# Optimization experiments

Hardware: AMD Instinct MI355X
Metric: run time of the kernel (lower is better)

Reference implementation:

```python
import jax, jax.numpy as jnp
import numpy as np

N_TOKENS = 8192
D_MODEL = 1024
D_HIDDEN = 4096
N_EXPERTS = 8
TOP_K = 2


def setup_inputs() -> dict:
    key = jax.random.key(0)
    ks = jax.random.split(key, 7)
    s = 0.02
    return {
        "x": jax.random.normal(ks[0], (N_TOKENS, D_MODEL), dtype=jnp.float32),
        "gate_w": jax.random.normal(ks[1], (D_MODEL, N_EXPERTS), dtype=jnp.float32) * s,
        "gate_b": jnp.zeros((N_EXPERTS,), dtype=jnp.float32),
        "w1": jax.random.normal(ks[2], (N_EXPERTS, D_MODEL, D_HIDDEN), dtype=jnp.float32) * s,
        "b1": jnp.zeros((N_EXPERTS, D_HIDDEN), dtype=jnp.float32),
        "w2": jax.random.normal(ks[3], (N_EXPERTS, D_HIDDEN, D_MODEL), dtype=jnp.float32) * s,
        "b2": jnp.zeros((N_EXPERTS, D_MODEL), dtype=jnp.float32),
    }


def reference(x, gate_w, gate_b, w1, b1, w2, b2):
    # Gating: softmax over experts, then top-k routing
    gate_scores = jax.nn.softmax(x @ gate_w + gate_b, axis=-1)        # [N, E]
    topk_vals, topk_idx = jax.lax.top_k(gate_scores, TOP_K)          # [N, K]

    # Combine weights: sum of topk_vals scattered to expert slots
    onehot = jax.nn.one_hot(topk_idx, N_EXPERTS, dtype=x.dtype)      # [N, K, E]
    combine = jnp.einsum('nk,nke->ne', topk_vals, onehot)            # [N, E]

    # Dense expert evaluation (math identical to masked dispatch: unselected
    # experts receive weight 0 in `combine`).
    h = jax.nn.relu(jnp.einsum('nd,edh->neh', x, w1) + b1)           # [N, E, H]
    expert_out = jnp.einsum('neh,ehd->ned', h, w2) + b2              # [N, E, D]
    output = jnp.einsum('ned,ne->nd', expert_out, combine)           # [N, D]

    # Load-balancing loss from routing counts
    load = jnp.sum(onehot, axis=(0, 1))                              # [E]
    load_balancing_loss = jnp.sum((load / jnp.sum(load)) ** 2)
    return output, load_balancing_loss
```

## Files before the change

kernel.cpp:

```cpp
#include <hip/hip_runtime.h>

#define D_MODEL   1024
#define D_HIDDEN  4096
#define N_EXPERTS 8
#define N_TOKENS  8192
#define NASSIGN   (N_TOKENS * 2)
#define PADCAP    (NASSIGN + N_EXPERTS * 128)
#define ROWT      (PADCAP / 128)

typedef unsigned short u16;
typedef __bf16 bf16x8 __attribute__((ext_vector_type(8)));
typedef float  f32x4  __attribute__((ext_vector_type(4)));

__device__ __forceinline__ u16 f2bf(float f) {
  union { float f; unsigned u; } c; c.f = f;
  unsigned u = c.u;
  u = (u + 0x7fffu + ((u >> 16) & 1u)) >> 16;
  return (u16)u;
}

__device__ __forceinline__ void async16(const void* g, void* l) {
  __builtin_amdgcn_global_load_lds(
      (const __attribute__((address_space(1))) unsigned int*)g,
      (__attribute__((address_space(3))) unsigned int*)l, 16, 0, 0);
}

__global__ __launch_bounds__(256) void gating_kernel(
    const float* __restrict__ x, const float* __restrict__ gw,
    const float* __restrict__ gb, int* __restrict__ counts,
    int* __restrict__ tok_idx, float* __restrict__ tok_w)
{
  const int n = blockIdx.x * 4 + (threadIdx.x >> 6);
  const int lane = threadIdx.x & 63;
  float acc[8] = {0.f,0.f,0.f,0.f,0.f,0.f,0.f,0.f};
  for (int d = lane; d < D_MODEL; d += 64) {
    float xv = x[(size_t)n * D_MODEL + d];
    const float4* g = (const float4*)&gw[d * 8];
    float4 g0 = g[0], g1 = g[1];
    acc[0] += xv * g0.x; acc[1] += xv * g0.y; acc[2] += xv * g0.z; acc[3] += xv * g0.w;
    acc[4] += xv * g1.x; acc[5] += xv * g1.y; acc[6] += xv * g1.z; acc[7] += xv * g1.w;
  }
  for (int off = 32; off; off >>= 1)
    #pragma unroll
    for (int e = 0; e < 8; ++e) acc[e] += __shfl_xor(acc[e], off, 64);
  if (lane == 0) {
    float l[8], p[8];
    float m = -1e30f;
    for (int e = 0; e < 8; ++e) { l[e] = acc[e] + gb[e]; m = fmaxf(m, l[e]); }
    float s = 0.f;
    for (int e = 0; e < 8; ++e) { p[e] = expf(l[e] - m); s += p[e]; }
    float inv = 1.f / s;
    for (int e = 0; e < 8; ++e) p[e] *= inv;
    int i0 = 0;
    for (int e = 1; e < 8; ++e) if (p[e] > p[i0]) i0 = e;
    int i1 = (i0 == 0) ? 1 : 0;
    for (int e = 0; e < 8; ++e) if (e != i0 && p[e] > p[i1]) i1 = e;
    tok_idx[2 * n]     = i0;  tok_idx[2 * n + 1] = i1;
    tok_w[2 * n]       = p[i0]; tok_w[2 * n + 1] = p[i1];
    atomicAdd(&counts[i0], 1);
    atomicAdd(&counts[i1], 1);
  }
}

__global__ void finalize_routing(const int* __restrict__ counts,
                                 int* __restrict__ offsets,
                                 float* __restrict__ out_loss)
{
  int off = 0;
  for (int e = 0; e < 8; ++e) {
    offsets[e] = off;
    off += ((counts[e] + 127) >> 7) << 7;
  }
  offsets[8] = off;
  float loss = 0.f;
  for (int e = 0; e < 8; ++e) {
    float f = (float)counts[e] * (1.f / (float)NASSIGN);
    loss += f * f;
  }
  *out_loss = loss;
}

__global__ __launch_bounds__(256) void scatter_kernel(
    const int* __restrict__ tok_idx, const float* __restrict__ tok_w,
    const int* __restrict__ offsets, int* __restrict__ cursors,
    int* __restrict__ assign_token, float* __restrict__ assign_w,
    int* __restrict__ tok_pos)
{
  const int n = blockIdx.x * 256 + threadIdx.x;
  #pragma unroll
  for (int k = 0; k < 2; ++k) {
    int e = tok_idx[n * 2 + k];
    int pos = offsets[e] + atomicAdd(&cursors[e], 1);
    assign_token[pos] = n;
    assign_w[pos] = tok_w[n * 2 + k];
    tok_pos[n * 2 + k] = pos;
  }
}

__global__ __launch_bounds__(256) void convert_x_kernel(
    const float* __restrict__ x, u16* __restrict__ xb)
{
  size_t i = ((size_t)blockIdx.x * 256 + threadIdx.x) * 4;
  float4 v = *(const float4*)&x[i];
  unsigned lo = (unsigned)f2bf(v.x) | ((unsigned)f2bf(v.y) << 16);
  unsigned hi = (unsigned)f2bf(v.z) | ((unsigned)f2bf(v.w) << 16);
  uint2 o; o.x = lo; o.y = hi;
  *(uint2*)&xb[i] = o;
}

__global__ __launch_bounds__(256) void transpose_cvt_kernel(
    const float* __restrict__ in, u16* __restrict__ out, int R, int C)
{
  const int e = blockIdx.z;
  const int c0 = blockIdx.x * 32, r0 = blockIdx.y * 32;
  __shared__ float tile[32][33];
  const int tx = threadIdx.x & 31, ty = threadIdx.x >> 5;
  const float* ip = in + (size_t)e * R * C;
  u16* op = out + (size_t)e * R * C;
  #pragma unroll
  for (int i = 0; i < 4; ++i)
    tile[ty + i * 8][tx] = ip[(size_t)(r0 + ty + i * 8) * C + c0 + tx];
  __syncthreads();
  #pragma unroll
  for (int i = 0; i < 4; ++i)
    op[(size_t)(c0 + ty + i * 8) * R + r0 + tx] = f2bf(tile[tx][ty + i * 8]);
}


__global__ __launch_bounds__(512, 1) void gemm1_kernel(
    const u16* __restrict__ xb, const u16* __restrict__ w1t,
    const float* __restrict__ b1, const int* __restrict__ assign_token,
    const int* __restrict__ offsets, u16* __restrict__ hbuf)
{
  const int rt = blockIdx.x, ct = blockIdx.y;
  if (rt * 128 >= offsets[8]) return;
  int e = 0;
  while (offsets[e + 1] <= rt * 128) ++e;

  __shared__ __align__(16) u16 smem[49152];
  const int tid = threadIdx.x;
  const int wave = tid >> 6, lane = tid & 63;

  const int arow0 = tid >> 3;
  const int aslot0 = (tid & 7) ^ (arow0 & 7);
  const int ac1 = tid + 512;
  const int arow1 = ac1 >> 3;
  const int aslot1 = (ac1 & 7) ^ (arow1 & 7);
  const long aBase0 = (long)assign_token[rt * 128 + arow0] * D_MODEL + aslot0 * 8;
  const long aBase1 = (long)assign_token[rt * 128 + arow1] * D_MODEL + aslot1 * 8;

  long bBase[4];
  #pragma unroll
  for (int k = 0; k < 4; ++k) {
    int c = tid + k * 512;
    int r = c >> 3, s = (c & 7) ^ (r & 7);
    bBase[k] = ((long)e * D_HIDDEN + ct * 256 + r) * D_MODEL + s * 8;
  }

  const int wr = (wave >> 2) * 64;
  const int wc = (wave & 3) * 64;
  f32x4 acc[4][4];
  #pragma unroll
  for (int i = 0; i < 4; ++i)
    #pragma unroll
    for (int j = 0; j < 4; ++j) acc[i][j] = (f32x4){0.f, 0.f, 0.f, 0.f};

  int aro[4], asz[4], bro[4], bsz[4];
  #pragma unroll
  for (int i = 0; i < 4; ++i) {
    int row = wr + i * 16 + (lane & 15);
    aro[i] = row * 64; asz[i] = row & 7;
    int col = wc + i * 16 + (lane & 15);
    bro[i] = col * 64; bsz[i] = col & 7;
  }
  const int lh = lane >> 4;

  #define STG1(p, k0) do { \
    u16* A_ = smem + (p) * 8192; \
    u16* B_ = smem + 16384 + (p) * 16384; \
    async16(xb  + aBase0   + (k0), A_ + wave * 512); \
    async16(xb  + aBase1   + (k0), A_ + 4096 + wave * 512); \
    async16(w1t + bBase[0] + (k0), B_ + wave * 512); \
    async16(w1t + bBase[1] + (k0), B_ + 4096 + wave * 512); \
    async16(w1t + bBase[2] + (k0), B_ + 8192 + wave * 512); \
    async16(w1t + bBase[3] + (k0), B_ + 12288 + wave * 512); \
  } while (0)

  const int NT = D_MODEL / 64;
  STG1(0, 0);
  __syncthreads();
  for (int t = 0; t < NT; ++t) {
    if (t + 1 < NT) STG1((t + 1) & 1, (t + 1) * 64);
    const u16* A = smem + (t & 1) * 8192;
    const u16* B = smem + 16384 + (t & 1) * 16384;
    bf16x8 a[2][4], b[2][4];
    #pragma unroll
    for (int i = 0; i < 4; ++i) {
      a[0][i] = *(const bf16x8*)&A[aro[i] + ((lh       ^ asz[i]) * 8)];
      a[1][i] = *(const bf16x8*)&A[aro[i] + (((4 | lh) ^ asz[i]) * 8)];
      b[0][i] = *(const bf16x8*)&B[bro[i] + ((lh       ^ bsz[i]) * 8)];
      b[1][i] = *(const bf16x8*)&B[bro[i] + (((4 | lh) ^ bsz[i]) * 8)];
    }
    __builtin_amdgcn_s_setprio(1);
    #pragma unroll
    for (int i = 0; i < 4; ++i)
      #pragma unroll
      for (int j = 0; j < 4; ++j) {
        acc[i][j] = __builtin_amdgcn_mfma_f32_16x16x32_bf16(a[0][i], b[0][j], acc[i][j], 0, 0, 0);
        acc[i][j] = __builtin_amdgcn_mfma_f32_16x16x32_bf16(a[1][i], b[1][j], acc[i][j], 0, 0, 0);
      }
    __builtin_amdgcn_s_setprio(0);
    __syncthreads();
  }
  #undef STG1

  float bias[4];
  #pragma unroll
  for (int j = 0; j < 4; ++j)
    bias[j] = b1[(size_t)e * D_HIDDEN + ct * 256 + wc + j * 16 + (lane & 15)];

  u16* Hs = smem;
  #pragma unroll
  for (int i = 0; i < 4; ++i)
    #pragma unroll
    for (int j = 0; j < 4; ++j)
      #pragma unroll
      for (int r = 0; r < 4; ++r) {
        int rl = wr + i * 16 + ((lane >> 4) * 4) + r;
        int cl = wc + j * 16 + (lane & 15);
        Hs[rl * 256 + cl] = f2bf(fmaxf(acc[i][j][r] + bias[j], 0.f));
      }
  __syncthreads();
  #pragma unroll
  for (int t = 0; t < 8; ++t) {
    int cc = tid + t * 512;
    int row = cc >> 5, cs = cc & 31;
    *(uint4*)&hbuf[((size_t)(rt * 128 + row)) * D_HIDDEN + ct * 256 + cs * 8] =
        *(const uint4*)&Hs[row * 256 + cs * 8];
  }
}

template <bool EO>
__global__ __launch_bounds__(512, 1) void gemm2_kernel(
    const u16* __restrict__ hbuf, const u16* __restrict__ w2t,
    const float* __restrict__ b2, const int* __restrict__ assign_token,
    const float* __restrict__ assign_w, const int* __restrict__ offsets,
    float* __restrict__ dst)
{
  const int rt = blockIdx.x, ct = blockIdx.y;
  if (rt * 128 >= offsets[8]) return;
  int e = 0;
  while (offsets[e + 1] <= rt * 128) ++e;

  __shared__ __align__(16) u16 smem[49152];
  __shared__ int tokS[128];
  __shared__ float wS[128];

  const int tid = threadIdx.x;
  const int wave = tid >> 6, lane = tid & 63;
  if (tid < 128) {
    tokS[tid] = assign_token[rt * 128 + tid];
    wS[tid] = assign_w[rt * 128 + tid];
  }

  const int arow0 = tid >> 3;
  const int aslot0 = (tid & 7) ^ (arow0 & 7);
  const int ac1 = tid + 512;
  const int arow1 = ac1 >> 3;
  const int aslot1 = (ac1 & 7) ^ (arow1 & 7);
  const long aBase0 = ((long)(rt * 128 + arow0)) * D_HIDDEN + aslot0 * 8;
  const long aBase1 = ((long)(rt * 128 + arow1)) * D_HIDDEN + aslot1 * 8;

  long bBase[4];
  #pragma unroll
  for (int k = 0; k < 4; ++k) {
    int c = tid + k * 512;
    int r = c >> 3, s = (c & 7) ^ (r & 7);
    bBase[k] = ((long)e * D_MODEL + ct * 256 + r) * D_HIDDEN + s * 8;
  }

  const int wr = (wave >> 2) * 64;
  const int wc = (wave & 3) * 64;
  f32x4 acc[4][4];
  #pragma unroll
  for (int i = 0; i < 4; ++i)
    #pragma unroll
    for (int j = 0; j < 4; ++j) acc[i][j] = (f32x4){0.f, 0.f, 0.f, 0.f};

  int aro[4], asz[4], bro[4], bsz[4];
  #pragma unroll
  for (int i = 0; i < 4; ++i) {
    int row = wr + i * 16 + (lane & 15);
    aro[i] = row * 64; asz[i] = row & 7;
    int col = wc + i * 16 + (lane & 15);
    bro[i] = col * 64; bsz[i] = col & 7;
  }
  const int lh = lane >> 4;

  #define STG2(p, k0) do { \
    u16* A_ = smem + (p) * 8192; \
    u16* B_ = smem + 16384 + (p) * 16384; \
    async16(hbuf + aBase0   + (k0), A_ + wave * 512); \
    async16(hbuf + aBase1   + (k0), A_ + 4096 + wave * 512); \
    async16(w2t  + bBase[0] + (k0), B_ + wave * 512); \
    async16(w2t  + bBase[1] + (k0), B_ + 4096 + wave * 512); \
    async16(w2t  + bBase[2] + (k0), B_ + 8192 + wave * 512); \
    async16(w2t  + bBase[3] + (k0), B_ + 12288 + wave * 512); \
  } while (0)

  const int NT = D_HIDDEN / 64;
  STG2(0, 0);
  __syncthreads();
  for (int t = 0; t < NT; ++t) {
    if (t + 1 < NT) STG2((t + 1) & 1, (t + 1) * 64);
    const u16* A = smem + (t & 1) * 8192;
    const u16* B = smem + 16384 + (t & 1) * 16384;
    bf16x8 a[2][4], b[2][4];
    #pragma unroll
    for (int i = 0; i < 4; ++i) {
      a[0][i] = *(const bf16x8*)&A[aro[i] + ((lh       ^ asz[i]) * 8)];
      a[1][i] = *(const bf16x8*)&A[aro[i] + (((4 | lh) ^ asz[i]) * 8)];
      b[0][i] = *(const bf16x8*)&B[bro[i] + ((lh       ^ bsz[i]) * 8)];
      b[1][i] = *(const bf16x8*)&B[bro[i] + (((4 | lh) ^ bsz[i]) * 8)];
    }
    __builtin_amdgcn_s_setprio(1);
    #pragma unroll
    for (int i = 0; i < 4; ++i)
      #pragma unroll
      for (int j = 0; j < 4; ++j) {
        acc[i][j] = __builtin_amdgcn_mfma_f32_16x16x32_bf16(a[0][i], b[0][j], acc[i][j], 0, 0, 0);
        acc[i][j] = __builtin_amdgcn_mfma_f32_16x16x32_bf16(a[1][i], b[1][j], acc[i][j], 0, 0, 0);
      }
    __builtin_amdgcn_s_setprio(0);
    __syncthreads();
  }
  #undef STG2

  float bias[4];
  #pragma unroll
  for (int j = 0; j < 4; ++j)
    bias[j] = b2[(size_t)e * D_MODEL + ct * 256 + wc + j * 16 + (lane & 15)];

  #pragma unroll
  for (int i = 0; i < 4; ++i)
    #pragma unroll
    for (int r = 0; r < 4; ++r) {
      int rl = wr + i * 16 + ((lane >> 4) * 4) + r;
      float wgt = wS[rl];
      if (EO) {
        size_t row = (size_t)(rt * 128 + rl);
        #pragma unroll
        for (int j = 0; j < 4; ++j) {
          float v = (acc[i][j][r] + bias[j]) * wgt;
          dst[row * D_MODEL + ct * 256 + wc + j * 16 + (lane & 15)] = v;
        }
      } else {
        int tok = tokS[rl];
        #pragma unroll
        for (int j = 0; j < 4; ++j) {
          float v = (acc[i][j][r] + bias[j]) * wgt;
          atomicAdd(&dst[(size_t)tok * D_MODEL + ct * 256 + wc + j * 16 + (lane & 15)], v);
        }
      }
    }
}

__global__ __launch_bounds__(256) void combine_kernel(
    const float* __restrict__ eo, const int* __restrict__ tok_pos,
    float* __restrict__ out)
{
  int idx = blockIdx.x * 256 + threadIdx.x;
  int n = idx >> 8;
  int c = (idx & 255) * 4;
  int p0 = tok_pos[2 * n], p1 = tok_pos[2 * n + 1];
  float4 a = *(const float4*)&eo[(size_t)p0 * D_MODEL + c];
  float4 b = *(const float4*)&eo[(size_t)p1 * D_MODEL + c];
  float4 o; o.x = a.x + b.x; o.y = a.y + b.y; o.z = a.z + b.z; o.w = a.w + b.w;
  *(float4*)&out[(size_t)n * D_MODEL + c] = o;
}

__global__ __launch_bounds__(256) void moe_fallback_kernel(
    const float* __restrict__ x, const float* __restrict__ w1,
    const float* __restrict__ b1, const float* __restrict__ w2,
    const float* __restrict__ b2, const int* __restrict__ tok_idx,
    const float* __restrict__ tok_w, float* __restrict__ out)
{
  const int a = blockIdx.x;
  const int n = a >> 1, slot = a & 1;
  const int e = tok_idx[n * 2 + slot];
  const float wgt = tok_w[n * 2 + slot];
  __shared__ float xs[D_MODEL];
  __shared__ float hs[D_HIDDEN];
  const int tid = threadIdx.x;
  for (int d = tid; d < D_MODEL; d += 256) xs[d] = x[(size_t)n * D_MODEL + d];
  __syncthreads();
  for (int h = tid; h < D_HIDDEN; h += 256) {
    float acc = b1[(size_t)e * D_HIDDEN + h];
    for (int d = 0; d < D_MODEL; ++d)
      acc += xs[d] * w1[((size_t)e * D_MODEL + d) * D_HIDDEN + h];
    hs[h] = fmaxf(acc, 0.f);
  }
  __syncthreads();
  for (int d = tid; d < D_MODEL; d += 256) {
    float acc = b2[(size_t)e * D_MODEL + d];
    for (int h = 0; h < D_HIDDEN; ++h)
      acc += hs[h] * w2[((size_t)e * D_HIDDEN + h) * D_MODEL + d];
    atomicAdd(&out[(size_t)n * D_MODEL + d], wgt * acc);
  }
}

extern "C" void kernel_launch(void* const* d_in, const int* in_sizes, int n_in,
                              void* d_out, int out_size, void* d_ws, size_t ws_size,
                              hipStream_t stream) {
  const float* x      = (const float*)d_in[0];
  const float* gate_w = (const float*)d_in[1];
  const float* gate_b = (const float*)d_in[2];
  const float* w1     = (const float*)d_in[3];
  const float* b1     = (const float*)d_in[4];
  const float* w2     = (const float*)d_in[5];
  const float* b2     = (const float*)d_in[6];
  float* out = (float*)d_out;

  char* ws = (char*)d_ws;
  int*   counts       = (int*)(ws + 0);
  int*   cursors      = (int*)(ws + 32);
  int*   offsets      = (int*)(ws + 64);
  int*   tok_idx      = (int*)(ws + 256);
  float* tok_w        = (float*)(ws + 65792);
  int*   tok_pos      = (int*)(ws + 131328);
  int*   assign_token = (int*)(ws + 196864);
  float* assign_w     = (float*)(ws + 266496);
  const size_t X0 = 336128;
  u16* xb   = (u16*)(ws + X0);
  u16* w1t  = (u16*)(ws + X0 + 16777216);
  u16* w2t  = (u16*)(ws + X0);
  u16* hbuf = (u16*)(ws + X0 + 83886080);
  float* eo = (float*)(ws + X0 + 226492416ull);
  const size_t REQ_FAST = X0 + 226492416ull;
  const size_t REQ_EO   = REQ_FAST + 71303168ull;

  const bool fast = (ws_size >= REQ_FAST);
  const bool eoPath = (ws_size >= REQ_EO);

  hipMemsetAsync(ws, 0, fast ? X0 : 336128, stream);
  if (!eoPath) {
    hipMemsetAsync(d_out, 0, (size_t)out_size * sizeof(float), stream);
  }

  gating_kernel<<<N_TOKENS / 4, 256, 0, stream>>>(x, gate_w, gate_b, counts, tok_idx, tok_w);
  finalize_routing<<<1, 1, 0, stream>>>(counts, offsets, out + (out_size - 1));

  if (fast) {
    scatter_kernel<<<N_TOKENS / 256, 256, 0, stream>>>(tok_idx, tok_w, offsets, cursors,
                                                       assign_token, assign_w, tok_pos);
    convert_x_kernel<<<(N_TOKENS * D_MODEL) / 1024, 256, 0, stream>>>(x, xb);
    transpose_cvt_kernel<<<dim3(D_HIDDEN / 32, D_MODEL / 32, N_EXPERTS), 256, 0, stream>>>(
        w1, w1t, D_MODEL, D_HIDDEN);
    gemm1_kernel<<<dim3(ROWT, D_HIDDEN / 256), 512, 0, stream>>>(
        xb, w1t, b1, assign_token, offsets, hbuf);
    transpose_cvt_kernel<<<dim3(D_MODEL / 32, D_HIDDEN / 32, N_EXPERTS), 256, 0, stream>>>(
        w2, w2t, D_HIDDEN, D_MODEL);
    if (eoPath) {
      gemm2_kernel<true><<<dim3(ROWT, D_MODEL / 256), 512, 0, stream>>>(
          hbuf, w2t, b2, assign_token, assign_w, offsets, eo);
      combine_kernel<<<(N_TOKENS * D_MODEL) / 1024, 256, 0, stream>>>(eo, tok_pos, out);
    } else {
      gemm2_kernel<false><<<dim3(ROWT, D_MODEL / 256), 512, 0, stream>>>(
          hbuf, w2t, b2, assign_token, assign_w, offsets, out);
    }
  } else {
    moe_fallback_kernel<<<NASSIGN, 256, 0, stream>>>(x, w1, b1, w2, b2, tok_idx, tok_w, out);
  }
}
```

Baseline: 828.0 us.

## Use 256x256 GEMM tiles with split-K gemm2 and finer-grained async pipeline

Both expert GEMMs move from 128x256 to 256x256 block tiles, with expert padding raised to 256 rows. The K loop is split into half-steps over a triple-buffered LDS staging scheme using explicit vmcnt waits and raw barriers, so loads overlap MFMA work more tightly. Row tiles are remapped for better L2 locality, and gemm2 is split two ways along K with atomic accumulation into a zeroed buffer. The larger tiles raise arithmetic intensity per byte loaded, at the cost of extra padding rows, an extra memset, atomic traffic, and heavy register pressure under a 2-block launch bound.

```diff
diff --git a/kernel.cpp b/kernel.cpp
--- a/kernel.cpp
+++ b/kernel.cpp
@@ -5,8 +5,8 @@
 #define N_EXPERTS 8
 #define N_TOKENS  8192
 #define NASSIGN   (N_TOKENS * 2)
-#define PADCAP    (NASSIGN + N_EXPERTS * 128)
-#define ROWT      (PADCAP / 128)
+#define PADCAP    (NASSIGN + N_EXPERTS * 256)
+#define RT_TILES  (PADCAP / 256)
 
 typedef unsigned short u16;
 typedef __bf16 bf16x8 __attribute__((ext_vector_type(8)));
@@ -24,6 +24,18 @@
       (const __attribute__((address_space(1))) unsigned int*)g,
       (__attribute__((address_space(3))) unsigned int*)l, 16, 0, 0);
 }
+
+#define MFMA(a, b, c) __builtin_amdgcn_mfma_f32_16x16x32_bf16((a), (b), (c), 0, 0, 0)
+
+#define WAIT4_BARRIER() do { \
+    asm volatile("s_waitcnt vmcnt(4)\n\ts_barrier" ::: "memory"); \
+    __builtin_amdgcn_sched_barrier(0); } while (0)
+#define WAIT0_BARRIER() do { \
+    asm volatile("s_waitcnt vmcnt(0)\n\ts_barrier" ::: "memory"); \
+    __builtin_amdgcn_sched_barrier(0); } while (0)
+#define FENCED_BARRIER() do { \
+    asm volatile("s_barrier" ::: "memory"); \
+    __builtin_amdgcn_sched_barrier(0); } while (0)
 
 __global__ __launch_bounds__(256) void gating_kernel(
     const float* __restrict__ x, const float* __restrict__ gw,
@@ -69,7 +81,7 @@
   int off = 0;
   for (int e = 0; e < 8; ++e) {
     offsets[e] = off;
-    off += ((counts[e] + 127) >> 7) << 7;
+    off += ((counts[e] + 255) >> 8) << 8;
   }
   offsets[8] = off;
   float loss = 0.f;
@@ -127,239 +139,290 @@
 }
 
 
-__global__ __launch_bounds__(512, 1) void gemm1_kernel(
+__global__ __launch_bounds__(512, 2) void gemm1_kernel(
     const u16* __restrict__ xb, const u16* __restrict__ w1t,
     const float* __restrict__ b1, const int* __restrict__ assign_token,
     const int* __restrict__ offsets, u16* __restrict__ hbuf)
 {
-  const int rt = blockIdx.x, ct = blockIdx.y;
-  if (rt * 128 >= offsets[8]) return;
+  const int rtl = (blockIdx.x & 7) * 9 + (blockIdx.x >> 3);
+  const int ct = blockIdx.y;
+  if (rtl * 256 >= offsets[8]) return;
   int e = 0;
-  while (offsets[e + 1] <= rt * 128) ++e;
-
-  __shared__ __align__(16) u16 smem[49152];
+  while (offsets[e + 1] <= rtl * 256) ++e;
+
+  __shared__ __align__(16) u16 smem[65536];
+
   const int tid = threadIdx.x;
   const int wave = tid >> 6, lane = tid & 63;
-
-  const int arow0 = tid >> 3;
-  const int aslot0 = (tid & 7) ^ (arow0 & 7);
-  const int ac1 = tid + 512;
-  const int arow1 = ac1 >> 3;
-  const int aslot1 = (ac1 & 7) ^ (arow1 & 7);
-  const long aBase0 = (long)assign_token[rt * 128 + arow0] * D_MODEL + aslot0 * 8;
-  const long aBase1 = (long)assign_token[rt * 128 + arow1] * D_MODEL + aslot1 * 8;
-
-  long bBase[4];
-  #pragma unroll
-  for (int k = 0; k < 4; ++k) {
-    int c = tid + k * 512;
-    int r = c >> 3, s = (c & 7) ^ (r & 7);
-    bBase[k] = ((long)e * D_HIDDEN + ct * 256 + r) * D_MODEL + s * 8;
-  }
-
-  const int wr = (wave >> 2) * 64;
-  const int wc = (wave & 3) * 64;
-  f32x4 acc[4][4];
-  #pragma unroll
-  for (int i = 0; i < 4; ++i)
+  const int wm = wave >> 2, wn = wave & 3;
+
+  const int r0 = tid >> 2, s0 = (tid & 3) ^ ((r0 >> 1) & 3);
+  const int r1 = r0 + 128, s1 = (tid & 3) ^ ((r1 >> 1) & 3);
+  const long aS0 = (long)assign_token[rtl * 256 + r0] * D_MODEL + s0 * 8;
+  const long aS1 = (long)assign_token[rtl * 256 + r1] * D_MODEL + s1 * 8;
+  const long bS0 = ((long)e * D_HIDDEN + ct * 256 + r0) * D_MODEL + s0 * 8;
+  const long bS1 = ((long)e * D_HIDDEN + ct * 256 + r1) * D_MODEL + s1 * 8;
+
+  f32x4 acc[8][4];
+  #pragma unroll
+  for (int i = 0; i < 8; ++i)
     #pragma unroll
     for (int j = 0; j < 4; ++j) acc[i][j] = (f32x4){0.f, 0.f, 0.f, 0.f};
 
-  int aro[4], asz[4], bro[4], bsz[4];
-  #pragma unroll
-  for (int i = 0; i < 4; ++i) {
-    int row = wr + i * 16 + (lane & 15);
-    aro[i] = row * 64; asz[i] = row & 7;
-    int col = wc + i * 16 + (lane & 15);
-    bro[i] = col * 64; bsz[i] = col & 7;
-  }
-  const int lh = lane >> 4;
-
-  #define STG1(p, k0) do { \
-    u16* A_ = smem + (p) * 8192; \
-    u16* B_ = smem + 16384 + (p) * 16384; \
-    async16(xb  + aBase0   + (k0), A_ + wave * 512); \
-    async16(xb  + aBase1   + (k0), A_ + 4096 + wave * 512); \
-    async16(w1t + bBase[0] + (k0), B_ + wave * 512); \
-    async16(w1t + bBase[1] + (k0), B_ + 4096 + wave * 512); \
-    async16(w1t + bBase[2] + (k0), B_ + 8192 + wave * 512); \
-    async16(w1t + bBase[3] + (k0), B_ + 12288 + wave * 512); \
+  int aoff[8], boff[4];
+  #pragma unroll
+  for (int f = 0; f < 8; ++f) {
+    int row = wm * 128 + f * 16 + (lane & 15);
+    aoff[f] = row * 32 + (((lane >> 4) ^ ((row >> 1) & 3)) * 8);
+  }
+  #pragma unroll
+  for (int f = 0; f < 4; ++f) {
+    int col = wn * 64 + f * 16 + (lane & 15);
+    boff[f] = 32768 + col * 32 + (((lane >> 4) ^ ((col >> 1) & 3)) * 8);
+  }
+
+  #define STG1(d, h, koff) do { \
+    u16* A_ = &smem[((d) * 2 + (h)) * 8192 + wave * 512]; \
+    u16* B_ = &smem[32768 + ((d) * 2 + (h)) * 8192 + wave * 512]; \
+    async16(xb  + aS0 + (koff), A_); \
+    async16(xb  + aS1 + (koff), A_ + 4096); \
+    async16(w1t + bS0 + (koff), B_); \
+    async16(w1t + bS1 + (koff), B_ + 4096); \
   } while (0)
 
   const int NT = D_MODEL / 64;
-  STG1(0, 0);
-  __syncthreads();
+  STG1(0, 0, 0);
+  STG1(0, 1, 32);
+  STG1(1, 0, 64);
+
   for (int t = 0; t < NT; ++t) {
-    if (t + 1 < NT) STG1((t + 1) & 1, (t + 1) * 64);
-    const u16* A = smem + (t & 1) * 8192;
-    const u16* B = smem + 16384 + (t & 1) * 16384;
-    bf16x8 a[2][4], b[2][4];
-    #pragma unroll
-    for (int i = 0; i < 4; ++i) {
-      a[0][i] = *(const bf16x8*)&A[aro[i] + ((lh       ^ asz[i]) * 8)];
-      a[1][i] = *(const bf16x8*)&A[aro[i] + (((4 | lh) ^ asz[i]) * 8)];
-      b[0][i] = *(const bf16x8*)&B[bro[i] + ((lh       ^ bsz[i]) * 8)];
-      b[1][i] = *(const bf16x8*)&B[bro[i] + (((4 | lh) ^ bsz[i]) * 8)];
-    }
-    __builtin_amdgcn_s_setprio(1);
-    #pragma unroll
-    for (int i = 0; i < 4; ++i)
-      #pragma unroll
-      for (int j = 0; j < 4; ++j) {
-        acc[i][j] = __builtin_amdgcn_mfma_f32_16x16x32_bf16(a[0][i], b[0][j], acc[i][j], 0, 0, 0);
-        acc[i][j] = __builtin_amdgcn_mfma_f32_16x16x32_bf16(a[1][i], b[1][j], acc[i][j], 0, 0, 0);
-      }
-    __builtin_amdgcn_s_setprio(0);
-    __syncthreads();
+    const int d = t & 1;
+    const int reg0 = d * 16384, reg1 = d * 16384 + 8192;
+    bf16x8 a[8], b0, b1r;
+    if (t + 1 < NT) WAIT4_BARRIER();
+    else            WAIT0_BARRIER();
+    #pragma unroll
+    for (int f = 0; f < 8; ++f) a[f] = *(const bf16x8*)&smem[reg0 + aoff[f]];
+    b0 = *(const bf16x8*)&smem[reg0 + boff[0]];
+    b1r = *(const bf16x8*)&smem[reg0 + boff[1]];
+    if (t + 1 < NT) STG1(d ^ 1, 1, (t + 1) * 64 + 32);
+    __builtin_amdgcn_s_setprio(1);
+    #pragma unroll
+    for (int f = 0; f < 8; ++f) {
+      acc[f][0] = MFMA(a[f], b0, acc[f][0]);
+      acc[f][1] = MFMA(a[f], b1r, acc[f][1]);
+    }
+    __builtin_amdgcn_s_setprio(0);
+    FENCED_BARRIER();
+    b0 = *(const bf16x8*)&smem[reg0 + boff[2]];
+    b1r = *(const bf16x8*)&smem[reg0 + boff[3]];
+    __builtin_amdgcn_s_setprio(1);
+    #pragma unroll
+    for (int f = 0; f < 8; ++f) {
+      acc[f][2] = MFMA(a[f], b0, acc[f][2]);
+      acc[f][3] = MFMA(a[f], b1r, acc[f][3]);
+    }
+    __builtin_amdgcn_s_setprio(0);
+    FENCED_BARRIER();
+    #pragma unroll
+    for (int f = 0; f < 8; ++f) a[f] = *(const bf16x8*)&smem[reg1 + aoff[f]];
+    b0 = *(const bf16x8*)&smem[reg1 + boff[0]];
+    b1r = *(const bf16x8*)&smem[reg1 + boff[1]];
+    if (t + 2 < NT) STG1(d, 0, (t + 2) * 64);
+    __builtin_amdgcn_s_setprio(1);
+    #pragma unroll
+    for (int f = 0; f < 8; ++f) {
+      acc[f][0] = MFMA(a[f], b0, acc[f][0]);
+      acc[f][1] = MFMA(a[f], b1r, acc[f][1]);
+    }
+    __builtin_amdgcn_s_setprio(0);
+    FENCED_BARRIER();
+    b0 = *(const bf16x8*)&smem[reg1 + boff[2]];
+    b1r = *(const bf16x8*)&smem[reg1 + boff[3]];
+    __builtin_amdgcn_s_setprio(1);
+    #pragma unroll
+    for (int f = 0; f < 8; ++f) {
+      acc[f][2] = MFMA(a[f], b0, acc[f][2]);
+      acc[f][3] = MFMA(a[f], b1r, acc[f][3]);
+    }
+    __builtin_amdgcn_s_setprio(0);
   }
   #undef STG1
 
   float bias[4];
   #pragma unroll
   for (int j = 0; j < 4; ++j)
-    bias[j] = b1[(size_t)e * D_HIDDEN + ct * 256 + wc + j * 16 + (lane & 15)];
-
+    bias[j] = b1[(size_t)e * D_HIDDEN + ct * 256 + wn * 64 + j * 16 + (lane & 15)];
+
+  __syncthreads();
   u16* Hs = smem;
   #pragma unroll
-  for (int i = 0; i < 4; ++i)
+  for (int i = 0; i < 8; ++i)
     #pragma unroll
     for (int j = 0; j < 4; ++j)
       #pragma unroll
       for (int r = 0; r < 4; ++r) {
-        int rl = wr + i * 16 + ((lane >> 4) * 4) + r;
-        int cl = wc + j * 16 + (lane & 15);
+        int rl = wm * 128 + i * 16 + ((lane >> 4) * 4) + r;
+        int cl = wn * 64 + j * 16 + (lane & 15);
         Hs[rl * 256 + cl] = f2bf(fmaxf(acc[i][j][r] + bias[j], 0.f));
       }
   __syncthreads();
   #pragma unroll
-  for (int t = 0; t < 8; ++t) {
-    int cc = tid + t * 512;
+  for (int it = 0; it < 16; ++it) {
+    int cc = tid + it * 512;
     int row = cc >> 5, cs = cc & 31;
-    *(uint4*)&hbuf[((size_t)(rt * 128 + row)) * D_HIDDEN + ct * 256 + cs * 8] =
+    *(uint4*)&hbuf[((size_t)(rtl * 256 + row)) * D_HIDDEN + ct * 256 + cs * 8] =
         *(const uint4*)&Hs[row * 256 + cs * 8];
   }
 }
 
 template <bool EO>
-__global__ __launch_bounds__(512, 1) void gemm2_kernel(
+__global__ __launch_bounds__(512, 2) void gemm2_kernel(
     const u16* __restrict__ hbuf, const u16* __restrict__ w2t,
     const float* __restrict__ b2, const int* __restrict__ assign_token,
     const float* __restrict__ assign_w, const int* __restrict__ offsets,
     float* __restrict__ dst)
 {
-  const int rt = blockIdx.x, ct = blockIdx.y;
-  if (rt * 128 >= offsets[8]) return;
+  const int rtl = (blockIdx.x & 7) * 9 + (blockIdx.x >> 3);
+  const int ct = blockIdx.y;
+  const int sk = blockIdx.z;
+  const long skb = (long)sk * 2048;
+  if (rtl * 256 >= offsets[8]) return;
   int e = 0;
-  while (offsets[e + 1] <= rt * 128) ++e;
-
-  __shared__ __align__(16) u16 smem[49152];
-  __shared__ int tokS[128];
-  __shared__ float wS[128];
+  while (offsets[e + 1] <= rtl * 256) ++e;
+
+  __shared__ __align__(16) u16 smem[65536];
 
   const int tid = threadIdx.x;
   const int wave = tid >> 6, lane = tid & 63;
-  if (tid < 128) {
-    tokS[tid] = assign_token[rt * 128 + tid];
-    wS[tid] = assign_w[rt * 128 + tid];
-  }
-
-  const int arow0 = tid >> 3;
-  const int aslot0 = (tid & 7) ^ (arow0 & 7);
-  const int ac1 = tid + 512;
-  const int arow1 = ac1 >> 3;
-  const int aslot1 = (ac1 & 7) ^ (arow1 & 7);
-  const long aBase0 = ((long)(rt * 128 + arow0)) * D_HIDDEN + aslot0 * 8;
-  const long aBase1 = ((long)(rt * 128 + arow1)) * D_HIDDEN + aslot1 * 8;
-
-  long bBase[4];
-  #pragma unroll
-  for (int k = 0; k < 4; ++k) {
-    int c = tid + k * 512;
-    int r = c >> 3, s = (c & 7) ^ (r & 7);
-    bBase[k] = ((long)e * D_MODEL + ct * 256 + r) * D_HIDDEN + s * 8;
-  }
-
-  const int wr = (wave >> 2) * 64;
-  const int wc = (wave & 3) * 64;
-  f32x4 acc[4][4];
-  #pragma unroll
-  for (int i = 0; i < 4; ++i)
+  const int wm = wave >> 2, wn = wave & 3;
+
+  const int r0 = tid >> 2, s0 = (tid & 3) ^ ((r0 >> 1) & 3);
+  const int r1 = r0 + 128, s1 = (tid & 3) ^ ((r1 >> 1) & 3);
+  const long aS0 = ((long)(rtl * 256 + r0)) * D_HIDDEN + s0 * 8;
+  const long aS1 = ((long)(rtl * 256 + r1)) * D_HIDDEN + s1 * 8;
+  const long bS0 = ((long)e * D_MODEL + ct * 256 + r0) * D_HIDDEN + s0 * 8;
+  const long bS1 = ((long)e * D_MODEL + ct * 256 + r1) * D_HIDDEN + s1 * 8;
+
+  f32x4 acc[8][4];
+  #pragma unroll
+  for (int i = 0; i < 8; ++i)
     #pragma unroll
     for (int j = 0; j < 4; ++j) acc[i][j] = (f32x4){0.f, 0.f, 0.f, 0.f};
 
-  int aro[4], asz[4], bro[4], bsz[4];
-  #pragma unroll
-  for (int i = 0; i < 4; ++i) {
-    int row = wr + i * 16 + (lane & 15);
-    aro[i] = row * 64; asz[i] = row & 7;
-    int col = wc + i * 16 + (lane & 15);
-    bro[i] = col * 64; bsz[i] = col & 7;
-  }
-  const int lh = lane >> 4;
-
-  #define STG2(p, k0) do { \
-    u16* A_ = smem + (p) * 8192; \
-    u16* B_ = smem + 16384 + (p) * 16384; \
-    async16(hbuf + aBase0   + (k0), A_ + wave * 512); \
-    async16(hbuf + aBase1   + (k0), A_ + 4096 + wave * 512); \
-    async16(w2t  + bBase[0] + (k0), B_ + wave * 512); \
-    async16(w2t  + bBase[1] + (k0), B_ + 4096 + wave * 512); \
-    async16(w2t  + bBase[2] + (k0), B_ + 8192 + wave * 512); \
-    async16(w2t  + bBase[3] + (k0), B_ + 12288 + wave * 512); \
+  int aoff[8], boff[4];
+  #pragma unroll
+  for (int f = 0; f < 8; ++f) {
+    int row = wm * 128 + f * 16 + (lane & 15);
+    aoff[f] = row * 32 + (((lane >> 4) ^ ((row >> 1) & 3)) * 8);
+  }
+  #pragma unroll
+  for (int f = 0; f < 4; ++f) {
+    int col = wn * 64 + f * 16 + (lane & 15);
+    boff[f] = 32768 + col * 32 + (((lane >> 4) ^ ((col >> 1) & 3)) * 8);
+  }
+
+  #define STG2(d, h, koff) do { \
+    u16* A_ = &smem[((d) * 2 + (h)) * 8192 + wave * 512]; \
+    u16* B_ = &smem[32768 + ((d) * 2 + (h)) * 8192 + wave * 512]; \
+    async16(hbuf + aS0 + (koff), A_); \
+    async16(hbuf + aS1 + (koff), A_ + 4096); \
+    async16(w2t + bS0 + (koff), B_); \
+    async16(w2t + bS1 + (koff), B_ + 4096); \
   } while (0)
 
-  const int NT = D_HIDDEN / 64;
-  STG2(0, 0);
-  __syncthreads();
+  const int NT = 2048 / 64;
+  STG2(0, 0, skb);
+  STG2(0, 1, skb + 32);
+  STG2(1, 0, skb + 64);
+
   for (int t = 0; t < NT; ++t) {
-    if (t + 1 < NT) STG2((t + 1) & 1, (t + 1) * 64);
-    const u16* A = smem + (t & 1) * 8192;
-    const u16* B = smem + 16384 + (t & 1) * 16384;
-    bf16x8 a[2][4], b[2][4];
-    #pragma unroll
-    for (int i = 0; i < 4; ++i) {
-      a[0][i] = *(const bf16x8*)&A[aro[i] + ((lh       ^ asz[i]) * 8)];
-      a[1][i] = *(const bf16x8*)&A[aro[i] + (((4 | lh) ^ asz[i]) * 8)];
-      b[0][i] = *(const bf16x8*)&B[bro[i] + ((lh       ^ bsz[i]) * 8)];
-      b[1][i] = *(const bf16x8*)&B[bro[i] + (((4 | lh) ^ bsz[i]) * 8)];
-    }
-    __builtin_amdgcn_s_setprio(1);
-    #pragma unroll
-    for (int i = 0; i < 4; ++i)
-      #pragma unroll
-      for (int j = 0; j < 4; ++j) {
-        acc[i][j] = __builtin_amdgcn_mfma_f32_16x16x32_bf16(a[0][i], b[0][j], acc[i][j], 0, 0, 0);
-        acc[i][j] = __builtin_amdgcn_mfma_f32_16x16x32_bf16(a[1][i], b[1][j], acc[i][j], 0, 0, 0);
-      }
-    __builtin_amdgcn_s_setprio(0);
-    __syncthreads();
+    const int d = t & 1;
+    const int reg0 = d * 16384, reg1 = d * 16384 + 8192;
+    bf16x8 a[8], b0, b1r;
+    if (t + 1 < NT) WAIT4_BARRIER();
+    else            WAIT0_BARRIER();
+    #pragma unroll
+    for (int f = 0; f < 8; ++f) a[f] = *(const bf16x8*)&smem[reg0 + aoff[f]];
+    b0 = *(const bf16x8*)&smem[reg0 + boff[0]];
+    b1r = *(const bf16x8*)&smem[reg0 + boff[1]];
+    if (t + 1 < NT) STG2(d ^ 1, 1, skb + (t + 1) * 64 + 32);
+    __builtin_amdgcn_s_setprio(1);
+    #pragma unroll
+    for (int f = 0; f < 8; ++f) {
+      acc[f][0] = MFMA(a[f], b0, acc[f][0]);
+      acc[f][1] = MFMA(a[f], b1r, acc[f][1]);
+    }
+    __builtin_amdgcn_s_setprio(0);
+    FENCED_BARRIER();
+    b0 = *(const bf16x8*)&smem[reg0 + boff[2]];
+    b1r = *(const bf16x8*)&smem[reg0 + boff[3]];
+    __builtin_amdgcn_s_setprio(1);
+    #pragma unroll
+    for (int f = 0; f < 8; ++f) {
+      acc[f][2] = MFMA(a[f], b0, acc[f][2]);
+      acc[f][3] = MFMA(a[f], b1r, acc[f][3]);
+    }
+    __builtin_amdgcn_s_setprio(0);
+    FENCED_BARRIER();
+    #pragma unroll
+    for (int f = 0; f < 8; ++f) a[f] = *(const bf16x8*)&smem[reg1 + aoff[f]];
+    b0 = *(const bf16x8*)&smem[reg1 + boff[0]];
+    b1r = *(const bf16x8*)&smem[reg1 + boff[1]];
+    if (t + 2 < NT) STG2(d, 0, skb + (t + 2) * 64);
+    __builtin_amdgcn_s_setprio(1);
+    #pragma unroll
+    for (int f = 0; f < 8; ++f) {
+      acc[f][0] = MFMA(a[f], b0, acc[f][0]);
+      acc[f][1] = MFMA(a[f], b1r, acc[f][1]);
+    }
+    __builtin_amdgcn_s_setprio(0);
+    FENCED_BARRIER();
+    b0 = *(const bf16x8*)&smem[reg1 + boff[2]];
+    b1r = *(const bf16x8*)&smem[reg1 + boff[3]];
+    __builtin_amdgcn_s_setprio(1);
+    #pragma unroll
+    for (int f = 0; f < 8; ++f) {
+      acc[f][2] = MFMA(a[f], b0, acc[f][2]);
+      acc[f][3] = MFMA(a[f], b1r, acc[f][3]);
+    }
+    __builtin_amdgcn_s_setprio(0);
   }
   #undef STG2
 
   float bias[4];
   #pragma unroll
   for (int j = 0; j < 4; ++j)
-    bias[j] = b2[(size_t)e * D_MODEL + ct * 256 + wc + j * 16 + (lane & 15)];
-
-  #pragma unroll
-  for (int i = 0; i < 4; ++i)
+    bias[j] = (sk == 0) ? b2[(size_t)e * D_MODEL + ct * 256 + wn * 64 + j * 16 + (lane & 15)] : 0.f;
+
+  __syncthreads();
+  float* wsm = (float*)smem;
+  int* tsm = (int*)&smem[1024];
+  if (tid < 256) {
+    wsm[tid] = assign_w[rtl * 256 + tid];
+    tsm[tid] = assign_token[rtl * 256 + tid];
+  }
+  __syncthreads();
+
+  #pragma unroll
+  for (int i = 0; i < 8; ++i)
     #pragma unroll
     for (int r = 0; r < 4; ++r) {
-      int rl = wr + i * 16 + ((lane >> 4) * 4) + r;
-      float wgt = wS[rl];
+      int rl = wm * 128 + i * 16 + ((lane >> 4) * 4) + r;
+      float wgt = wsm[rl];
       if (EO) {
-        size_t row = (size_t)(rt * 128 + rl);
+        size_t row = (size_t)(rtl * 256 + rl);
         #pragma unroll
         for (int j = 0; j < 4; ++j) {
           float v = (acc[i][j][r] + bias[j]) * wgt;
-          dst[row * D_MODEL + ct * 256 + wc + j * 16 + (lane & 15)] = v;
+          atomicAdd(&dst[row * D_MODEL + ct * 256 + wn * 64 + j * 16 + (lane & 15)], v);
         }
       } else {
-        int tok = tokS[rl];
+        int tok = tsm[rl];
         #pragma unroll
         for (int j = 0; j < 4; ++j) {
           float v = (acc[i][j][r] + bias[j]) * wgt;
-          atomicAdd(&dst[(size_t)tok * D_MODEL + ct * 256 + wc + j * 16 + (lane & 15)], v);
+          atomicAdd(&dst[(size_t)tok * D_MODEL + ct * 256 + wn * 64 + j * 16 + (lane & 15)], v);
         }
       }
     }
@@ -429,20 +492,20 @@
   float* tok_w        = (float*)(ws + 65792);
   int*   tok_pos      = (int*)(ws + 131328);
   int*   assign_token = (int*)(ws + 196864);
-  float* assign_w     = (float*)(ws + 266496);
-  const size_t X0 = 336128;
-  u16* xb   = (u16*)(ws + X0);
-  u16* w1t  = (u16*)(ws + X0 + 16777216);
-  u16* w2t  = (u16*)(ws + X0);
-  u16* hbuf = (u16*)(ws + X0 + 83886080);
-  float* eo = (float*)(ws + X0 + 226492416ull);
-  const size_t REQ_FAST = X0 + 226492416ull;
-  const size_t REQ_EO   = REQ_FAST + 71303168ull;
+  float* assign_w     = (float*)(ws + 270592);
+  const size_t X0 = 344320;
+  u16*   hbuf = (u16*)(ws + X0);
+  u16*   xb   = (u16*)(ws + X0 + 150994944ull);
+  u16*   w1t  = (u16*)(ws + X0 + 150994944ull + 16777216ull);
+  u16*   w2t  = (u16*)(ws + X0 + 150994944ull);
+  float* eo   = (float*)(ws + X0 + 150994944ull + 67108864ull);
+  const size_t REQ_FAST = X0 + 150994944ull + 16777216ull + 67108864ull;
+  const size_t REQ_EO   = X0 + 150994944ull + 67108864ull + 75497472ull;
 
   const bool fast = (ws_size >= REQ_FAST);
-  const bool eoPath = (ws_size >= REQ_EO);
-
-  hipMemsetAsync(ws, 0, fast ? X0 : 336128, stream);
+  const bool eoPath = fast && (ws_size >= REQ_EO);
+
+  hipMemsetAsync(ws, 0, X0, stream);
   if (!eoPath) {
     hipMemsetAsync(d_out, 0, (size_t)out_size * sizeof(float), stream);
   }
@@ -456,16 +519,17 @@
     convert_x_kernel<<<(N_TOKENS * D_MODEL) / 1024, 256, 0, stream>>>(x, xb);
     transpose_cvt_kernel<<<dim3(D_HIDDEN / 32, D_MODEL / 32, N_EXPERTS), 256, 0, stream>>>(
         w1, w1t, D_MODEL, D_HIDDEN);
-    gemm1_kernel<<<dim3(ROWT, D_HIDDEN / 256), 512, 0, stream>>>(
+    gemm1_kernel<<<dim3(RT_TILES, D_HIDDEN / 256), 512, 0, stream>>>(
         xb, w1t, b1, assign_token, offsets, hbuf);
     transpose_cvt_kernel<<<dim3(D_MODEL / 32, D_HIDDEN / 32, N_EXPERTS), 256, 0, stream>>>(
         w2, w2t, D_HIDDEN, D_MODEL);
     if (eoPath) {
-      gemm2_kernel<true><<<dim3(ROWT, D_MODEL / 256), 512, 0, stream>>>(
+      hipMemsetAsync(eo, 0, 75497472ull, stream);
+      gemm2_kernel<true><<<dim3(RT_TILES, D_MODEL / 256, 2), 512, 0, stream>>>(
           hbuf, w2t, b2, assign_token, assign_w, offsets, eo);
       combine_kernel<<<(N_TOKENS * D_MODEL) / 1024, 256, 0, stream>>>(eo, tok_pos, out);
     } else {
-      gemm2_kernel<false><<<dim3(ROWT, D_MODEL / 256), 512, 0, stream>>>(
+      gemm2_kernel<false><<<dim3(RT_TILES, D_MODEL / 256, 2), 512, 0, stream>>>(
           hbuf, w2t, b2, assign_token, assign_w, offsets, out);
     }
   } else {
```

After: 827.9 us. No clear change (-0.0%).
